# Kernel tuning notes

Hardware: AMD Instinct MI355X
Metric: run time of the kernel (lower is better)

## Reference

```python
import jax, jax.numpy as jnp
import numpy as np

B, N, D, H = 4, 1024, 1024, 16
HD = D // H
SCALE = HD ** -0.5


def setup_inputs() -> dict:
    key = jax.random.key(0)
    ks = jax.random.split(key, 12)
    s = 0.02
    return {
        "q": jax.random.normal(ks[0], (B, N, D), jnp.float32),
        "k": jax.random.normal(ks[1], (B, N, D), jnp.float32),
        "v": jax.random.normal(ks[2], (B, N, D), jnp.float32),
        "rel_pos_emb": jax.random.normal(ks[3], (N, N, HD), jnp.float32) * s,
        "Wq": jax.random.normal(ks[4], (D, D), jnp.float32) * s,
        "bq": jnp.zeros((D,), jnp.float32),
        "Wk": jax.random.normal(ks[5], (D, D), jnp.float32) * s,
        "bk": jnp.zeros((D,), jnp.float32),
        "Wv": jax.random.normal(ks[6], (D, D), jnp.float32) * s,
        "bv": jnp.zeros((D,), jnp.float32),
        "Wo": jax.random.normal(ks[7], (D, D), jnp.float32) * s,
        "bo": jnp.zeros((D,), jnp.float32),
    }


def reference(q, k, v, rel_pos_emb, Wq, bq, Wk, bk, Wv, bv, Wo, bo):
    # Linear projections (torch Linear: x @ W.T + b)
    qp = q @ Wq.T + bq
    kp = k @ Wk.T + bk
    vp = v @ Wv.T + bv
    # [b, n, (h d)] -> [b, h, n, d]
    split = lambda t: t.reshape(t.shape[0], t.shape[1], H, HD).transpose(0, 2, 1, 3)
    qh = split(qp) * SCALE
    kh = split(kp)
    vh = split(vp)
    # content scores + relative-position scores (rel_pos_emb is [q,k,d];
    # the b,h repeat in the original is a pure broadcast, folded into einsum)
    attn = jnp.einsum('bhqd,bhkd->bhqk', qh, kh)
    attn = attn + jnp.einsum('bhqd,qkd->bhqk', qh, rel_pos_emb)
    attn = jax.nn.softmax(attn, axis=-1)  # dropout p=0.0 (eval): identity
    out = jnp.einsum('bhqk,bhkd->bhqd', attn, vh)
    out = out.transpose(0, 2, 1, 3).reshape(B, N, D)  # [b,h,n,d] -> [b,n,(h d)]
    return out @ Wo.T + bo
```

## Files before the change

### kernel.cpp

```cpp
#include <hip/hip_runtime.h>
#include <hip/hip_bf16.h>

#define NB 4
#define SEQ 1024
#define DM 1024
#define NH 16
#define HD 64
#define QSCALE 0.125f
#define NTOK (NB*SEQ)

using f32x4  = __attribute__((ext_vector_type(4))) float;
using bf16x8 = __attribute__((ext_vector_type(8))) short;
using s16x4  = __attribute__((ext_vector_type(4))) short;

__device__ __forceinline__ short f2bf(float x){
  __hip_bfloat16 h = __float2bfloat16(x);
  return *reinterpret_cast<short*>(&h);
}
__device__ __forceinline__ float bf2f(short x){
  __hip_bfloat16 h; *reinterpret_cast<short*>(&h) = x;
  return __bfloat162float(h);
}

__device__ __forceinline__ void gld16(const void* g, void* l){
  __builtin_amdgcn_global_load_lds(
      (const __attribute__((address_space(1))) unsigned int*)g,
      (__attribute__((address_space(3))) unsigned int*)l, 16, 0, 0);
}

__global__ void cvt_all(const float* __restrict__ a0, const float* __restrict__ a1,
                        const float* __restrict__ a2, const float* __restrict__ a3,
                        const float* __restrict__ a4, const float* __restrict__ a5,
                        const float* __restrict__ a6,
                        short* o0, short* o1, short* o2, short* o3,
                        short* o4, short* o5, short* o6, int big4, int small4){
  int i = blockIdx.x * blockDim.x + threadIdx.x;
  int y = blockIdx.y;
  int n4 = (y < 3) ? big4 : small4;
  if (i >= n4) return;
  const float* in; short* out;
  if      (y == 0){ in = a0; out = o0; }
  else if (y == 1){ in = a1; out = o1; }
  else if (y == 2){ in = a2; out = o2; }
  else if (y == 3){ in = a3; out = o3; }
  else if (y == 4){ in = a4; out = o4; }
  else if (y == 5){ in = a5; out = o5; }
  else            { in = a6; out = o6; }
  float4 v = reinterpret_cast<const float4*>(in)[i];
  s16x4 o;
  o[0] = f2bf(v.x); o[1] = f2bf(v.y); o[2] = f2bf(v.z); o[3] = f2bf(v.w);
  reinterpret_cast<s16x4*>(out)[i] = o;
}

__global__ __launch_bounds__(256) void proj_gemm(
    const short* __restrict__ qb, const short* __restrict__ kb, const short* __restrict__ vb,
    const short* __restrict__ wqb, const short* __restrict__ wkb, const short* __restrict__ wvb,
    const float* __restrict__ bq, const float* __restrict__ bk, const float* __restrict__ bv,
    short* __restrict__ qhb, short* __restrict__ khb, short* __restrict__ vTb)
{
  __shared__ short As[128*32];
  __shared__ short Bs[128*32];
  const int t = threadIdx.x, w = t >> 6, l = t & 63, lr = l & 15, lg = l >> 4;
  const int wr = w >> 1, wc = w & 1;
  const int which = blockIdx.y >> 3;
  const short *A, *Bt;
  int m0, n0;
  if (which == 2){ A = wvb; Bt = vb; m0 = (blockIdx.y & 7)*128; n0 = blockIdx.x*128; }
  else if (which == 1){ A = kb; Bt = wkb; m0 = blockIdx.x*128; n0 = (blockIdx.y & 7)*128; }
  else { A = qb; Bt = wqb; m0 = blockIdx.x*128; n0 = (blockIdx.y & 7)*128; }
  f32x4 acc[4][4] = {};
  for (int k0 = 0; k0 < DM; k0 += 32){
    __syncthreads();
    #pragma unroll
    for (int i = 0; i < 2; ++i){
      int c = i*256 + t, row = c >> 2, sl = c & 3;
      gld16(A  + (size_t)(m0 + row)*DM + k0 + sl*8, &As[c*8]);
      gld16(Bt + (size_t)(n0 + row)*DM + k0 + sl*8, &Bs[c*8]);
    }
    __syncthreads();
    bf16x8 af[4], bfr[4];
    #pragma unroll
    for (int m = 0; m < 4; ++m)
      af[m] = *reinterpret_cast<const bf16x8*>(&As[(wr*64 + m*16 + lr)*32 + lg*8]);
    #pragma unroll
    for (int n = 0; n < 4; ++n)
      bfr[n] = *reinterpret_cast<const bf16x8*>(&Bs[(wc*64 + n*16 + lr)*32 + lg*8]);
    #pragma unroll
    for (int m = 0; m < 4; ++m)
      #pragma unroll
      for (int n = 0; n < 4; ++n)
        acc[m][n] = __builtin_amdgcn_mfma_f32_16x16x32_bf16(af[m], bfr[n], acc[m][n], 0, 0, 0);
  }
  #pragma unroll
  for (int m = 0; m < 4; ++m){
    int row = m0 + wr*64 + m*16 + lg*4;
    #pragma unroll
    for (int n = 0; n < 4; ++n){
      int col = n0 + wc*64 + n*16 + lr;
      #pragma unroll
      for (int e = 0; e < 4; ++e){
        if (which == 0)
          qhb[(size_t)(row + e)*DM + col] = f2bf((acc[m][n][e] + bq[col]) * QSCALE);
        else if (which == 1)
          khb[(size_t)(row + e)*DM + col] = f2bf(acc[m][n][e] + bk[col]);
        else
          vTb[(size_t)(row + e)*NTOK + col] = f2bf(acc[m][n][e] + bv[row + e]);
      }
    }
  }
}

__global__ __launch_bounds__(256) void out_gemm(const short* __restrict__ A,
    const short* __restrict__ Bt, const float* __restrict__ bias, float* __restrict__ out)
{
  __shared__ short As[128*32];
  __shared__ short Bs[128*32];
  const int t = threadIdx.x, w = t >> 6, l = t & 63, lr = l & 15, lg = l >> 4;
  const int wr = w >> 1, wc = w & 1;
  const int m0 = blockIdx.x*128, n0 = blockIdx.y*128;
  f32x4 acc[4][4] = {};
  for (int k0 = 0; k0 < DM; k0 += 32){
    __syncthreads();
    #pragma unroll
    for (int i = 0; i < 2; ++i){
      int c = i*256 + t, row = c >> 2, sl = c & 3;
      gld16(A  + (size_t)(m0 + row)*DM + k0 + sl*8, &As[c*8]);
      gld16(Bt + (size_t)(n0 + row)*DM + k0 + sl*8, &Bs[c*8]);
    }
    __syncthreads();
    bf16x8 af[4], bfr[4];
    #pragma unroll
    for (int m = 0; m < 4; ++m)
      af[m] = *reinterpret_cast<const bf16x8*>(&As[(wr*64 + m*16 + lr)*32 + lg*8]);
    #pragma unroll
    for (int n = 0; n < 4; ++n)
      bfr[n] = *reinterpret_cast<const bf16x8*>(&Bs[(wc*64 + n*16 + lr)*32 + lg*8]);
    #pragma unroll
    for (int m = 0; m < 4; ++m)
      #pragma unroll
      for (int n = 0; n < 4; ++n)
        acc[m][n] = __builtin_amdgcn_mfma_f32_16x16x32_bf16(af[m], bfr[n], acc[m][n], 0, 0, 0);
  }
  #pragma unroll
  for (int m = 0; m < 4; ++m){
    int row = m0 + wr*64 + m*16 + lg*4;
    #pragma unroll
    for (int n = 0; n < 4; ++n){
      int col = n0 + wc*64 + n*16 + lr;
      float bb = bias[col];
      #pragma unroll
      for (int e = 0; e < 4; ++e)
        out[(size_t)(row + e)*DM + col] = acc[m][n][e] + bb;
    }
  }
}

__global__ __launch_bounds__(256) void relscore2(const short* __restrict__ qh,
    const float* __restrict__ rel, short* __restrict__ Rs)
{
  __shared__ short At[64*72];
  __shared__ short Bs[64*72];
  const int t = threadIdx.x, w = t >> 6, l = t & 63, lr = l & 15, lg = l >> 4;
  const int q = blockIdx.x;
  #pragma unroll
  for (int i = 0; i < 2; ++i){
    int c = t + i*256;
    int row = c >> 3, off = (c & 7) * 8;
    int b = row >> 4, h = row & 15;
    uint4 v = *reinterpret_cast<const uint4*>(qh + ((size_t)(b*SEQ + q)*NH + h)*HD + off);
    *reinterpret_cast<uint4*>(&At[row*72 + off]) = v;
  }
  __syncthreads();
  bf16x8 af[2];
  af[0] = *reinterpret_cast<const bf16x8*>(&At[(w*16 + lr)*72 + lg*8]);
  af[1] = *reinterpret_cast<const bf16x8*>(&At[(w*16 + lr)*72 + 32 + lg*8]);
  for (int k0 = 0; k0 < SEQ; k0 += 64){
    __syncthreads();
    #pragma unroll
    for (int i = 0; i < 4; ++i){
      int c = t + i*256;
      int row = c >> 4, off = (c & 15) * 4;
      float4 v = *reinterpret_cast<const float4*>(rel + ((size_t)q*SEQ + k0 + row)*HD + off);
      s16x4 o;
      o[0] = f2bf(v.x); o[1] = f2bf(v.y); o[2] = f2bf(v.z); o[3] = f2bf(v.w);
      *reinterpret_cast<s16x4*>(&Bs[row*72 + off]) = o;
    }
    __syncthreads();
    f32x4 acc[4] = {};
    #pragma unroll
    for (int s = 0; s < 2; ++s){
      #pragma unroll
      for (int tt = 0; tt < 4; ++tt){
        bf16x8 bf = *reinterpret_cast<const bf16x8*>(&Bs[(tt*16 + lr)*72 + s*32 + lg*8]);
        acc[tt] = __builtin_amdgcn_mfma_f32_16x16x32_bf16(af[s], bf, acc[tt], 0, 0, 0);
      }
    }
    #pragma unroll
    for (int tt = 0; tt < 4; ++tt){
      #pragma unroll
      for (int e = 0; e < 4; ++e){
        int bh = w*16 + lg*4 + e;
        Rs[((size_t)q*64 + bh)*SEQ + k0 + tt*16 + lr] = f2bf(acc[tt][e]);
      }
    }
  }
}

__global__ __launch_bounds__(256) void flash2(const short* __restrict__ qh,
    const short* __restrict__ kh, const short* __restrict__ vT,
    const short* __restrict__ Rs, short* __restrict__ ao)
{
  __shared__ short Kt[128*64];
  __shared__ short Vt[64*128];
  __shared__ short Pt[64*136];
  const int t = threadIdx.x, w = t >> 6, l = t & 63, lr = l & 15, lg = l >> 4;
  const int bh = blockIdx.x, b = bh >> 4, h = bh & 15;
  const int q0 = blockIdx.y * 64;
  bf16x8 qf[2];
  {
    const short* qbase = qh + ((size_t)(b*SEQ + (q0 + w*16 + lr))*NH + h)*HD;
    qf[0] = *reinterpret_cast<const bf16x8*>(qbase + lg*8);
    qf[1] = *reinterpret_cast<const bf16x8*>(qbase + 32 + lg*8);
  }
  f32x4 oacc[4] = {};
  float lrow[4] = {0.f, 0.f, 0.f, 0.f};
  for (int kt = 0; kt < SEQ/128; ++kt){
    const int kbase = kt * 128;
    __syncthreads();
    #pragma unroll
    for (int i = 0; i < 4; ++i){
      int c = i*256 + t, row = c >> 3, sl = c & 7;
      gld16(kh + (size_t)(b*SEQ + kbase + row)*DM + h*HD + 8*(sl ^ (row & 7)), &Kt[c*8]);
    }
    #pragma unroll
    for (int i = 0; i < 4; ++i){
      int c = i*256 + t, row = c >> 4, sl = c & 15;
      gld16(vT + (size_t)(h*HD + row)*NTOK + b*SEQ + kbase + 8*(sl ^ (row & 15)), &Vt[c*8]);
    }
    f32x4 sa[8];
    #pragma unroll
    for (int tt = 0; tt < 8; ++tt)
      #pragma unroll
      for (int e = 0; e < 4; ++e){
        int row = q0 + w*16 + lg*4 + e;
        sa[tt][e] = bf2f(Rs[((size_t)row*64 + bh)*SEQ + kbase + tt*16 + lr]);
      }
    __syncthreads();
    #pragma unroll
    for (int s = 0; s < 2; ++s)
      #pragma unroll
      for (int tt = 0; tt < 8; ++tt){
        int krow = tt*16 + lr;
        bf16x8 kf = *reinterpret_cast<const bf16x8*>(&Kt[krow*64 + 8*((s*4 + lg) ^ (krow & 7))]);
        sa[tt] = __builtin_amdgcn_mfma_f32_16x16x32_bf16(qf[s], kf, sa[tt], 0, 0, 0);
      }
    float rs_[4] = {0.f, 0.f, 0.f, 0.f};
    #pragma unroll
    for (int tt = 0; tt < 8; ++tt)
      #pragma unroll
      for (int e = 0; e < 4; ++e){
        float p = __expf(sa[tt][e]);
        rs_[e] += p;
        Pt[(w*16 + lg*4 + e)*136 + tt*16 + lr] = f2bf(p);
      }
    #pragma unroll
    for (int e = 0; e < 4; ++e){
      #pragma unroll
      for (int mm = 1; mm < 16; mm <<= 1)
        rs_[e] += __shfl_xor(rs_[e], mm, 16);
      lrow[e] += rs_[e];
    }
    #pragma unroll
    for (int ks = 0; ks < 4; ++ks){
      bf16x8 pa = *reinterpret_cast<const bf16x8*>(&Pt[(w*16 + lr)*136 + ks*32 + lg*8]);
      #pragma unroll
      for (int tt = 0; tt < 4; ++tt){
        int vrow = tt*16 + lr;
        bf16x8 vf = *reinterpret_cast<const bf16x8*>(&Vt[vrow*128 + 8*((ks*4 + lg) ^ (vrow & 15))]);
        oacc[tt] = __builtin_amdgcn_mfma_f32_16x16x32_bf16(pa, vf, oacc[tt], 0, 0, 0);
      }
    }
  }
  #pragma unroll
  for (int tt = 0; tt < 4; ++tt){
    #pragma unroll
    for (int e = 0; e < 4; ++e){
      int q = q0 + w*16 + lg*4 + e;
      int hd = tt*16 + lr;
      ao[((size_t)(b*SEQ + q))*DM + h*HD + hd] = f2bf(oacc[tt][e] / lrow[e]);
    }
  }
}

extern "C" void kernel_launch(void* const* d_in, const int* in_sizes, int n_in,
                              void* d_out, int out_size, void* d_ws, size_t ws_size,
                              hipStream_t stream)
{
  const float* q   = (const float*)d_in[0];
  const float* k   = (const float*)d_in[1];
  const float* v   = (const float*)d_in[2];
  const float* rel = (const float*)d_in[3];
  const float* Wq  = (const float*)d_in[4];
  const float* bq  = (const float*)d_in[5];
  const float* Wk  = (const float*)d_in[6];
  const float* bk  = (const float*)d_in[7];
  const float* Wv  = (const float*)d_in[8];
  const float* bv  = (const float*)d_in[9];
  const float* Wo  = (const float*)d_in[10];
  const float* bo  = (const float*)d_in[11];
  float* out = (float*)d_out;

  char* ws = (char*)d_ws;
  short* qb  = (short*)(ws);
  short* kb  = (short*)(ws + 8388608);
  short* vb  = (short*)(ws + 16777216);
  short* qhb = (short*)(ws + 25165824);
  short* khb = (short*)(ws + 33554432);
  short* vTb = (short*)(ws + 41943040);
  short* aob = (short*)(ws + 50331648);
  short* wqb = (short*)(ws + 58720256);
  short* wkb = (short*)(ws + 60817408);
  short* wvb = (short*)(ws + 62914560);
  short* wob = (short*)(ws + 65011712);
  short* Rs  = (short*)(ws + 67108864);

  dim3 blk(256);
  {
    int big4 = NTOK*DM/4, small4 = DM*DM/4;
    cvt_all<<<dim3(big4/256, 7), blk, 0, stream>>>(q, k, v, Wq, Wk, Wv, Wo,
        qb, kb, vb, wqb, wkb, wvb, wob, big4, small4);
  }
  proj_gemm<<<dim3(NTOK/128, 24), blk, 0, stream>>>(qb, kb, vb, wqb, wkb, wvb,
      bq, bk, bv, qhb, khb, vTb);
  relscore2<<<dim3(SEQ), blk, 0, stream>>>(qhb, rel, Rs);
  flash2<<<dim3(NB*NH, SEQ/64), blk, 0, stream>>>(qhb, khb, vTb, Rs, aob);
  out_gemm<<<dim3(NTOK/128, DM/128), blk, 0, stream>>>(aob, wob, bo, out);
}
```

Baseline: 246.6 us.

## Rewrite relative-position score kernel to load operands straight into registers

The rel-score kernel drops its LDS staging and block-wide barriers. Each wave now loads its own 16-key slice of rel_pos_emb from global memory, converts it to bf16 in registers, and holds all 64 (b,h) query fragments in registers. It also swaps the MFMA operand roles so that each lane writes four contiguous bf16 scores as one 8-byte store, replacing scattered 2-byte stores. The aim is to remove barrier stalls and uncoalesced writes in this bandwidth-bound pass over the large fp32 rel tensor, at the cost of more registers per thread.

After: 257.6 us. 1.04x slower.

```diff
diff --git a/kernel.cpp b/kernel.cpp
--- a/kernel.cpp
+++ b/kernel.cpp
@@ -155,53 +155,41 @@
   }
 }
 
-__global__ __launch_bounds__(256) void relscore2(const short* __restrict__ qh,
+__global__ __launch_bounds__(256) void relscore3(const short* __restrict__ qh,
     const float* __restrict__ rel, short* __restrict__ Rs)
 {
-  __shared__ short At[64*72];
-  __shared__ short Bs[64*72];
   const int t = threadIdx.x, w = t >> 6, l = t & 63, lr = l & 15, lg = l >> 4;
   const int q = blockIdx.x;
+  bf16x8 qf[4][2];
   #pragma unroll
-  for (int i = 0; i < 2; ++i){
-    int c = t + i*256;
-    int row = c >> 3, off = (c & 7) * 8;
-    int b = row >> 4, h = row & 15;
-    uint4 v = *reinterpret_cast<const uint4*>(qh + ((size_t)(b*SEQ + q)*NH + h)*HD + off);
-    *reinterpret_cast<uint4*>(&At[row*72 + off]) = v;
-  }
-  __syncthreads();
-  bf16x8 af[2];
-  af[0] = *reinterpret_cast<const bf16x8*>(&At[(w*16 + lr)*72 + lg*8]);
-  af[1] = *reinterpret_cast<const bf16x8*>(&At[(w*16 + lr)*72 + 32 + lg*8]);
-  for (int k0 = 0; k0 < SEQ; k0 += 64){
-    __syncthreads();
-    #pragma unroll
-    for (int i = 0; i < 4; ++i){
-      int c = t + i*256;
-      int row = c >> 4, off = (c & 15) * 4;
-      float4 v = *reinterpret_cast<const float4*>(rel + ((size_t)q*SEQ + k0 + row)*HD + off);
-      s16x4 o;
-      o[0] = f2bf(v.x); o[1] = f2bf(v.y); o[2] = f2bf(v.z); o[3] = f2bf(v.w);
-      *reinterpret_cast<s16x4*>(&Bs[row*72 + off]) = o;
-    }
-    __syncthreads();
-    f32x4 acc[4] = {};
+  for (int n = 0; n < 4; ++n){
+    int bh = n*16 + lr, b = bh >> 4, h = bh & 15;
+    const short* base = qh + (size_t)(b*SEQ + q)*DM + h*HD;
+    qf[n][0] = *reinterpret_cast<const bf16x8*>(base + lg*8);
+    qf[n][1] = *reinterpret_cast<const bf16x8*>(base + 32 + lg*8);
+  }
+  for (int kt = w; kt < SEQ/16; kt += 4){
+    const int k0 = kt * 16;
+    bf16x8 rf[2];
     #pragma unroll
     for (int s = 0; s < 2; ++s){
-      #pragma unroll
-      for (int tt = 0; tt < 4; ++tt){
-        bf16x8 bf = *reinterpret_cast<const bf16x8*>(&Bs[(tt*16 + lr)*72 + s*32 + lg*8]);
-        acc[tt] = __builtin_amdgcn_mfma_f32_16x16x32_bf16(af[s], bf, acc[tt], 0, 0, 0);
-      }
-    }
-    #pragma unroll
-    for (int tt = 0; tt < 4; ++tt){
-      #pragma unroll
-      for (int e = 0; e < 4; ++e){
-        int bh = w*16 + lg*4 + e;
-        Rs[((size_t)q*64 + bh)*SEQ + k0 + tt*16 + lr] = f2bf(acc[tt][e]);
-      }
+      const float* rp = rel + ((size_t)q*SEQ + k0 + lr)*HD + s*32 + lg*8;
+      float4 v0 = *reinterpret_cast<const float4*>(rp);
+      float4 v1 = *reinterpret_cast<const float4*>(rp + 4);
+      bf16x8 o;
+      o[0]=f2bf(v0.x); o[1]=f2bf(v0.y); o[2]=f2bf(v0.z); o[3]=f2bf(v0.w);
+      o[4]=f2bf(v1.x); o[5]=f2bf(v1.y); o[6]=f2bf(v1.z); o[7]=f2bf(v1.w);
+      rf[s] = o;
+    }
+    #pragma unroll
+    for (int n = 0; n < 4; ++n){
+      f32x4 acc = {};
+      acc = __builtin_amdgcn_mfma_f32_16x16x32_bf16(rf[0], qf[n][0], acc, 0, 0, 0);
+      acc = __builtin_amdgcn_mfma_f32_16x16x32_bf16(rf[1], qf[n][1], acc, 0, 0, 0);
+      union { int2 i2; short s4[4]; } u;
+      u.s4[0] = f2bf(acc[0]); u.s4[1] = f2bf(acc[1]);
+      u.s4[2] = f2bf(acc[2]); u.s4[3] = f2bf(acc[3]);
+      *reinterpret_cast<int2*>(Rs + ((size_t)q*64 + n*16 + lr)*SEQ + k0 + lg*4) = u.i2;
     }
   }
 }
@@ -332,7 +320,7 @@
   }
   proj_gemm<<<dim3(NTOK/128, 24), blk, 0, stream>>>(qb, kb, vb, wqb, wkb, wvb,
       bq, bk, bv, qhb, khb, vTb);
-  relscore2<<<dim3(SEQ), blk, 0, stream>>>(qhb, rel, Rs);
+  relscore3<<<dim3(SEQ), blk, 0, stream>>>(qhb, rel, Rs);
   flash2<<<dim3(NB*NH, SEQ/64), blk, 0, stream>>>(qhb, khb, vTb, Rs, aob);
   out_gemm<<<dim3(NTOK/128, DM/128), blk, 0, stream>>>(aob, wob, bo, out);
 }
```
